# Performance work log

Hardware: AMD Instinct MI355X
Metric: run time of the kernel (lower is better)

## Reference

```python
import jax, jax.numpy as jnp
import numpy as np
from math import pi as PI

N_NODES = 50000
N_EDGES = 1000000
HIDDEN = 128
N_GAUSS = 50
N_FILT = 128
N_COLORS = 4
CUTOFF = 10.0
LOG2 = float(np.log(2.0))


def setup_inputs() -> dict:
    key = jax.random.key(0)
    ks = jax.random.split(key, 16)
    glorot = jax.nn.initializers.glorot_uniform()
    inp = {
        "x": jax.random.normal(ks[0], (N_NODES, HIDDEN), jnp.float32),
        "edge_index": jax.random.randint(ks[1], (2, N_EDGES), 0, N_NODES),
        "edge_weight": jax.random.uniform(ks[2], (N_EDGES,), jnp.float32) * CUTOFF,
        "edge_attr": jax.random.normal(ks[3], (N_EDGES, N_GAUSS), jnp.float32),
        "colors": jax.random.randint(ks[4], (N_EDGES,), 0, N_COLORS),
        # ColoredMLP params, stacked over colors
        "mlp1_w": glorot(ks[5], (N_COLORS, N_FILT, N_GAUSS), jnp.float32),
        "mlp1_b": jnp.zeros((N_COLORS, N_FILT), jnp.float32),
        "mlp2_w": glorot(ks[6], (N_COLORS, N_FILT, N_FILT), jnp.float32),
        "mlp2_b": jnp.zeros((N_COLORS, N_FILT), jnp.float32),
        # CFConv linears
        "lin1_w": glorot(ks[7], (N_FILT, HIDDEN), jnp.float32),
        "lin2_w": glorot(ks[8], (HIDDEN, N_FILT), jnp.float32),
        "lin2_b": jnp.zeros((HIDDEN,), jnp.float32),
        # final Linear
        "lin_w": glorot(ks[9], (HIDDEN, HIDDEN), jnp.float32),
        "lin_b": jnp.zeros((HIDDEN,), jnp.float32),
    }
    return inp


def shifted_softplus(v):
    return jax.nn.softplus(v) - LOG2


def colored_mlp(edge_attr, colors, mlp1_w, mlp1_b, mlp2_w, mlp2_b):
    # per-color small MLP; loop over the small fixed color set, select by mask
    out = jnp.zeros((edge_attr.shape[0], N_FILT), edge_attr.dtype)
    for c in range(N_COLORS):
        h = shifted_softplus(edge_attr @ mlp1_w[c].T + mlp1_b[c])
        h = h @ mlp2_w[c].T + mlp2_b[c]
        out = jnp.where((colors == c)[:, None], h, out)
    return out


def reference(x, edge_index, edge_weight, edge_attr, colors,
              mlp1_w, mlp1_b, mlp2_w, mlp2_b,
              lin1_w, lin2_w, lin2_b, lin_w, lin_b):
    # cosine cutoff
    C = 0.5 * (jnp.cos(edge_weight * PI / CUTOFF) + 1.0)  # [E]
    W = colored_mlp(edge_attr, colors, mlp1_w, mlp1_b, mlp2_w, mlp2_b) * C[:, None]  # [E,F]
    h = x @ lin1_w.T  # [N,F]
    src, dst = edge_index[0], edge_index[1]
    msg = h[src] * W  # gather + modulate, [E,F]
    agg = jax.ops.segment_sum(msg, dst, num_segments=N_NODES)  # scatter-add, [N,F]
    out = agg @ lin2_w.T + lin2_b  # [N,H]
    out = shifted_softplus(out)
    out = out @ lin_w.T + lin_b
    return out
```

## Files before the change

kernel.cpp:

```cpp
#include <hip/hip_runtime.h>
#include <math.h>

#define N_NODES_ 50000
#define N_EDGES_ 1000000
#define HID 128
#define NG 50
#define NF 128
#define NCOL 4
#define CSEG 258048
#define NKEY (NCOL * N_NODES_)
#define CHUNK 625
#define NCHUNK_PER_C 80
#define NCHUNK (NCOL * NCHUNK_PER_C)

typedef short s16x8 __attribute__((ext_vector_type(8)));
typedef float f32x4 __attribute__((ext_vector_type(4)));

__device__ __forceinline__ float sspf(float v) {
    float r = __logf(1.f + __expf(v)) - 0.69314718055994531f;
    return (v > 15.f) ? (v - 0.69314718055994531f) : r;
}

__device__ __forceinline__ unsigned int f2b(float f) {
    unsigned int u = __float_as_uint(f);
    return (u + 0x7fffu + ((u >> 16) & 1u)) >> 16;
}

__global__ __launch_bounds__(256) void hist_kernel(const int* __restrict__ colors,
                                                   const int* __restrict__ edge_index,
                                                   int* __restrict__ hist) {
    int e = blockIdx.x * 256 + threadIdx.x;
    if (e < N_EDGES_) {
        int key = colors[e] * N_NODES_ + edge_index[N_EDGES_ + e];
        atomicAdd(&hist[key], 1);
    }
}

__global__ __launch_bounds__(256) void scan1_kernel(int* __restrict__ hist,
                                                    int* __restrict__ csum) {
    __shared__ int s[CHUNK];
    int b = blockIdx.x;
    int c = b / NCHUNK_PER_C, ch = b % NCHUNK_PER_C;
    int gofs = c * N_NODES_ + ch * CHUNK;
    for (int i = threadIdx.x; i < CHUNK; i += 256) s[i] = hist[gofs + i];
    __syncthreads();
    if (threadIdx.x == 0) {
        int run = 0;
        for (int i = 0; i < CHUNK; ++i) { int t = s[i]; s[i] = run; run += t; }
        csum[b] = run;
    }
    __syncthreads();
    for (int i = threadIdx.x; i < CHUNK; i += 256) hist[gofs + i] = s[i];
}

__global__ __launch_bounds__(64) void scan2_kernel(const int* __restrict__ csum,
                                                   int* __restrict__ cbase,
                                                   int* __restrict__ g_cnt) {
    int c = threadIdx.x;
    if (c < NCOL) {
        int run = 0;
        for (int j = 0; j < NCHUNK_PER_C; ++j) {
            cbase[c * NCHUNK_PER_C + j] = run;
            run += csum[c * NCHUNK_PER_C + j];
        }
        g_cnt[c] = run;
    }
}

__global__ __launch_bounds__(256) void scan3_kernel(int* __restrict__ hist,
                                                    const int* __restrict__ cbase) {
    int b = blockIdx.x;
    int c = b / NCHUNK_PER_C, ch = b % NCHUNK_PER_C;
    int gofs = c * N_NODES_ + ch * CHUNK;
    int add = cbase[b];
    for (int i = threadIdx.x; i < CHUNK; i += 256) hist[gofs + i] += add;
}

__global__ __launch_bounds__(256) void scatter_kernel(const int* __restrict__ colors,
                                                      const int* __restrict__ edge_index,
                                                      const float* __restrict__ edge_weight,
                                                      int* __restrict__ base,
                                                      int* __restrict__ eid_s,
                                                      int* __restrict__ dst_s,
                                                      float* __restrict__ cw_s) {
    int e = blockIdx.x * 256 + threadIdx.x;
    if (e < N_EDGES_) {
        int c = colors[e];
        int d = edge_index[N_EDGES_ + e];
        int key = c * N_NODES_ + d;
        int r = atomicAdd(&base[key], 1);
        int slot = c * CSEG + r;
        eid_s[slot] = e;
        dst_s[slot] = d;
        cw_s[slot] = 0.5f * (__cosf(edge_weight[e] * 0.31415926535897932f) + 1.f);
    }
}

__global__ __launch_bounds__(256) void wconv_kernel(const float* __restrict__ m1w,
                                                    const float* __restrict__ m2w,
                                                    unsigned short* __restrict__ m1b16,
                                                    unsigned short* __restrict__ m2b16) {
    int idx = blockIdx.x * 256 + threadIdx.x;
    if (idx < NCOL * NF * 64) {
        int c = idx / (NF * 64);
        int rem = idx % (NF * 64);
        int n = rem / 64, k = rem % 64;
        float v = (k < NG) ? m1w[(c * NF + n) * NG + k] : 0.f;
        m1b16[idx] = (unsigned short)f2b(v);
    } else if (idx < NCOL * NF * 64 + NCOL * NF * NF) {
        int j = idx - NCOL * NF * 64;
        int cn = j / NF;
        int k = j % NF;
        int ks = k >> 5, qk = (k >> 3) & 3, jj = k & 7;
        int tau = ((2 * ks + (jj >> 2)) << 4) | (qk << 2) | (jj & 3);
        m2b16[j] = (unsigned short)f2b(m2w[cn * NF + tau]);
    }
}

__global__ __launch_bounds__(256, 4) void passA_kernel(
    const int* __restrict__ edge_index,
    const float* __restrict__ edge_attr,
    const unsigned short* __restrict__ m1b16, const unsigned short* __restrict__ m2b16,
    const float* __restrict__ m1bias, const float* __restrict__ m2bias,
    const float* __restrict__ h, const int* __restrict__ eid_s,
    const int* __restrict__ dst_s, const float* __restrict__ cw_s,
    const int* __restrict__ g_cnt, float* __restrict__ agg) {

    __shared__ __align__(16) char sm2[32768];

    int c = blockIdx.x >> 12;
    int tile = blockIdx.x & 4095;
    int cnt = g_cnt[c];
    if (tile * 64 >= cnt) return;
    int pos0 = c * CSEG + tile * 64;

    int tid = threadIdx.x;
    int wv = tid >> 6;
    int l15 = tid & 15;
    int q = (tid >> 4) & 3;
    int e = (wv << 4) | l15;

    {
        const uint4* g4 = (const uint4*)(m2b16 + (size_t)c * NF * NF);
#pragma unroll
        for (int i = 0; i < 8; ++i) {
            int c0 = tid + 256 * i;
            int row = c0 >> 4;
            int k0 = c0 & 15;
            int dstb = row * 256 + ((k0 * 16) ^ ((row & 7) << 4));
            *(uint4*)(sm2 + dstb) = g4[c0];
        }
    }

    int eid = eid_s[pos0 + e];
    int d = dst_s[pos0 + e];
    float cw = cw_s[pos0 + e];
    int sidx = 0;
    if (eid >= 0) sidx = edge_index[eid];

    union { s16x8 v; unsigned int u[4]; } bf0, bf1;
    {
        const float* ear = edge_attr + (size_t)((eid >= 0) ? eid : 0) * NG;
        float2 a0 = *(const float2*)(ear + q * 8 + 0);
        float2 a1 = *(const float2*)(ear + q * 8 + 2);
        float2 a2 = *(const float2*)(ear + q * 8 + 4);
        float2 a3 = *(const float2*)(ear + q * 8 + 6);
        bf0.u[0] = f2b(a0.x) | (f2b(a0.y) << 16);
        bf0.u[1] = f2b(a1.x) | (f2b(a1.y) << 16);
        bf0.u[2] = f2b(a2.x) | (f2b(a2.y) << 16);
        bf0.u[3] = f2b(a3.x) | (f2b(a3.y) << 16);
        float2 c0 = make_float2(0.f, 0.f), c1 = c0, c2 = c0, c3 = c0;
        int k1 = 32 + q * 8;
        if (q < 2) {
            c0 = *(const float2*)(ear + k1 + 0);
            c1 = *(const float2*)(ear + k1 + 2);
            c2 = *(const float2*)(ear + k1 + 4);
            c3 = *(const float2*)(ear + k1 + 6);
        } else if (q == 2) {
            c0 = *(const float2*)(ear + 48);
        }
        bf1.u[0] = f2b(c0.x) | (f2b(c0.y) << 16);
        bf1.u[1] = f2b(c1.x) | (f2b(c1.y) << 16);
        bf1.u[2] = f2b(c2.x) | (f2b(c2.y) << 16);
        bf1.u[3] = f2b(c3.x) | (f2b(c3.y) << 16);
    }

    uint2 p[8];
    {
        const unsigned short* m1p = m1b16 + (size_t)c * NF * 64;
        const float* b1p = m1bias + c * NF;
#pragma unroll
        for (int m = 0; m < 8; ++m) {
            f32x4 a = (f32x4)(0.f);
            s16x8 af0 = *(const s16x8*)(m1p + (m * 16 + l15) * 64 + q * 8);
            a = __builtin_amdgcn_mfma_f32_16x16x32_bf16(af0, bf0.v, a, 0, 0, 0);
            s16x8 af1 = *(const s16x8*)(m1p + (m * 16 + l15) * 64 + q * 8 + 32);
            a = __builtin_amdgcn_mfma_f32_16x16x32_bf16(af1, bf1.v, a, 0, 0, 0);
            int n0 = m * 16 + q * 4;
            f32x4 bv = *(const f32x4*)(b1p + n0);
            float t0 = sspf(a[0] + bv[0]);
            float t1 = sspf(a[1] + bv[1]);
            float t2 = sspf(a[2] + bv[2]);
            float t3 = sspf(a[3] + bv[3]);
            p[m].x = f2b(t0) | (f2b(t1) << 16);
            p[m].y = f2b(t2) | (f2b(t3) << 16);
        }
    }

    int dprev = __shfl_up(d, 1, 16);
    int dn1 = __shfl_down(d, 1, 16);
    int dn2 = __shfl_down(d, 2, 16);
    int dn4 = __shfl_down(d, 4, 16);
    int dn8 = __shfl_down(d, 8, 16);
    bool s1 = (dn1 == d) && (l15 + 1 < 16);
    bool s2 = (dn2 == d) && (l15 + 2 < 16);
    bool s4 = (dn4 == d) && (l15 + 4 < 16);
    bool s8 = (dn8 == d) && (l15 + 8 < 16);
    bool head = (d >= 0) && (l15 == 0 || d != dprev);

    __syncthreads();

    const float* b2p = m2bias + c * NF;
    const float* hrow = h + (size_t)sidx * HID;
    float* ap = agg + (size_t)((d >= 0) ? d : 0) * HID + (q << 2);
    int rowb0 = l15 * 256;
    int sw = (l15 & 7) << 4;

#pragma unroll
    for (int m = 0; m < 8; ++m) {
        f32x4 a2 = (f32x4)(0.f);
        const char* rp = sm2 + rowb0 + m * 4096;
#pragma unroll
        for (int ks = 0; ks < 4; ++ks) {
            union { s16x8 v; unsigned int u[4]; } bfr;
            bfr.u[0] = p[2 * ks].x;
            bfr.u[1] = p[2 * ks].y;
            bfr.u[2] = p[2 * ks + 1].x;
            bfr.u[3] = p[2 * ks + 1].y;
            s16x8 af = *(const s16x8*)(rp + ((q * 16 + ks * 64) ^ sw));
            a2 = __builtin_amdgcn_mfma_f32_16x16x32_bf16(af, bfr.v, a2, 0, 0, 0);
        }
        int n0 = m * 16 + q * 4;
        f32x4 hv = *(const f32x4*)(hrow + n0);
        f32x4 bv = *(const f32x4*)(b2p + n0);
        a2[0] = (a2[0] + bv[0]) * cw * hv[0];
        a2[1] = (a2[1] + bv[1]) * cw * hv[1];
        a2[2] = (a2[2] + bv[2]) * cw * hv[2];
        a2[3] = (a2[3] + bv[3]) * cw * hv[3];

#define SSTEP(sflag, dd)                                                     \
        {                                                                    \
            float v0 = __shfl_down(a2[0], dd, 16);                           \
            float v1 = __shfl_down(a2[1], dd, 16);                           \
            float v2 = __shfl_down(a2[2], dd, 16);                           \
            float v3 = __shfl_down(a2[3], dd, 16);                           \
            if (sflag) { a2[0] += v0; a2[1] += v1; a2[2] += v2; a2[3] += v3; } \
        }
        SSTEP(s1, 1)
        SSTEP(s2, 2)
        SSTEP(s4, 4)
        SSTEP(s8, 8)
#undef SSTEP

        if (head) {
            atomicAdd(ap + m * 16 + 0, a2[0]);
            atomicAdd(ap + m * 16 + 1, a2[1]);
            atomicAdd(ap + m * 16 + 2, a2[2]);
            atomicAdd(ap + m * 16 + 3, a2[3]);
        }
    }
}

__device__ __forceinline__ void fma_2x8(float (&acc)[2][8], float2 a, float4 b0, float4 b1) {
    acc[0][0] += a.x * b0.x; acc[0][1] += a.x * b0.y;
    acc[0][2] += a.x * b0.z; acc[0][3] += a.x * b0.w;
    acc[0][4] += a.x * b1.x; acc[0][5] += a.x * b1.y;
    acc[0][6] += a.x * b1.z; acc[0][7] += a.x * b1.w;
    acc[1][0] += a.y * b0.x; acc[1][1] += a.y * b0.y;
    acc[1][2] += a.y * b0.z; acc[1][3] += a.y * b0.w;
    acc[1][4] += a.y * b1.x; acc[1][5] += a.y * b1.y;
    acc[1][6] += a.y * b1.z; acc[1][7] += a.y * b1.w;
}

__device__ __forceinline__ void load_wT32(const float4* __restrict__ w4, int kc,
                                          float (*wT)[132], int tid) {
#pragma unroll
    for (int i = 0; i < 4; ++i) {
        int lin = tid + 256 * i;
        int col = lin >> 3;
        int m = lin & 7;
        float4 v = w4[col * 32 + (kc >> 2) + m];
        wT[4 * m + 0][col] = v.x;
        wT[4 * m + 1][col] = v.y;
        wT[4 * m + 2][col] = v.z;
        wT[4 * m + 3][col] = v.w;
    }
}

__global__ __launch_bounds__(256) void lin1_kernel(const float* __restrict__ x,
                                                   const float* __restrict__ w,
                                                   float* __restrict__ h) {
    __shared__ float xT[HID][36];
    __shared__ float wT[32][132];
    int tid = threadIdx.x;
    int tx = tid & 15, ty = tid >> 4;
    int r0 = blockIdx.x * 32;
    const float4* x4 = (const float4*)x;
#pragma unroll
    for (int i = 0; i < 4; ++i) {
        int lin = tid + 256 * i;
        int r = lin >> 5, m = lin & 31;
        int rr = r0 + r; if (rr > N_NODES_ - 1) rr = N_NODES_ - 1;
        float4 v = x4[rr * 32 + m];
        xT[4 * m + 0][r] = v.x; xT[4 * m + 1][r] = v.y;
        xT[4 * m + 2][r] = v.z; xT[4 * m + 3][r] = v.w;
    }
    float acc[2][8] = {};
    for (int kc = 0; kc < HID; kc += 32) {
        __syncthreads();
        load_wT32((const float4*)w, kc, wT, tid);
        __syncthreads();
#pragma unroll 8
        for (int k2 = 0; k2 < 32; ++k2) {
            float2 a = *(const float2*)&xT[kc + k2][2 * ty];
            float4 b0 = *(const float4*)&wT[k2][8 * tx];
            float4 b1 = *(const float4*)&wT[k2][8 * tx + 4];
            fma_2x8(acc, a, b0, b1);
        }
    }
    float4* h4 = (float4*)h;
#pragma unroll
    for (int i = 0; i < 2; ++i) {
        int row = r0 + 2 * ty + i;
        if (row < N_NODES_) {
            h4[row * 32 + 2 * tx]     = make_float4(acc[i][0], acc[i][1], acc[i][2], acc[i][3]);
            h4[row * 32 + 2 * tx + 1] = make_float4(acc[i][4], acc[i][5], acc[i][6], acc[i][7]);
        }
    }
}

__global__ __launch_bounds__(256) void out_kernel(
    const float* __restrict__ agg,
    const float* __restrict__ w2, const float* __restrict__ b2,
    const float* __restrict__ w3, const float* __restrict__ b3,
    float* __restrict__ out) {
    __shared__ float sT[HID][36];
    __shared__ float wT[32][132];
    int tid = threadIdx.x;
    int tx = tid & 15, ty = tid >> 4;
    int r0 = blockIdx.x * 32;
    const float4* a4 = (const float4*)agg;
#pragma unroll
    for (int i = 0; i < 4; ++i) {
        int lin = tid + 256 * i;
        int r = lin >> 5, m = lin & 31;
        int rr = r0 + r; if (rr > N_NODES_ - 1) rr = N_NODES_ - 1;
        float4 v = a4[rr * 32 + m];
        sT[4 * m + 0][r] = v.x; sT[4 * m + 1][r] = v.y;
        sT[4 * m + 2][r] = v.z; sT[4 * m + 3][r] = v.w;
    }
    float acc[2][8] = {};
    for (int kc = 0; kc < HID; kc += 32) {
        __syncthreads();
        load_wT32((const float4*)w2, kc, wT, tid);
        __syncthreads();
#pragma unroll 8
        for (int k2 = 0; k2 < 32; ++k2) {
            float2 a = *(const float2*)&sT[kc + k2][2 * ty];
            float4 c0 = *(const float4*)&wT[k2][8 * tx];
            float4 c1 = *(const float4*)&wT[k2][8 * tx + 4];
            fma_2x8(acc, a, c0, c1);
        }
    }
    __syncthreads();
#pragma unroll
    for (int j = 0; j < 8; ++j) {
        int col = 8 * tx + j;
        float bbv = b2[col];
        sT[col][2 * ty]     = sspf(acc[0][j] + bbv);
        sT[col][2 * ty + 1] = sspf(acc[1][j] + bbv);
    }
    float acc2[2][8] = {};
    for (int kc = 0; kc < HID; kc += 32) {
        __syncthreads();
        load_wT32((const float4*)w3, kc, wT, tid);
        __syncthreads();
#pragma unroll 8
        for (int k2 = 0; k2 < 32; ++k2) {
            float2 a = *(const float2*)&sT[kc + k2][2 * ty];
            float4 c0 = *(const float4*)&wT[k2][8 * tx];
            float4 c1 = *(const float4*)&wT[k2][8 * tx + 4];
            fma_2x8(acc2, a, c0, c1);
        }
    }
    float4* out4 = (float4*)out;
#pragma unroll
    for (int i = 0; i < 2; ++i) {
        int row = r0 + 2 * ty + i;
        if (row < N_NODES_) {
            out4[row * 32 + 2 * tx] = make_float4(
                acc2[i][0] + b3[8 * tx + 0], acc2[i][1] + b3[8 * tx + 1],
                acc2[i][2] + b3[8 * tx + 2], acc2[i][3] + b3[8 * tx + 3]);
            out4[row * 32 + 2 * tx + 1] = make_float4(
                acc2[i][4] + b3[8 * tx + 4], acc2[i][5] + b3[8 * tx + 5],
                acc2[i][6] + b3[8 * tx + 6], acc2[i][7] + b3[8 * tx + 7]);
        }
    }
}

extern "C" void kernel_launch(void* const* d_in, const int* in_sizes, int n_in,
                              void* d_out, int out_size, void* d_ws, size_t ws_size,
                              hipStream_t stream) {
    const float* x           = (const float*)d_in[0];
    const int*   edge_index  = (const int*)d_in[1];
    const float* edge_weight = (const float*)d_in[2];
    const float* edge_attr   = (const float*)d_in[3];
    const int*   colors      = (const int*)d_in[4];
    const float* m1w         = (const float*)d_in[5];
    const float* m1b         = (const float*)d_in[6];
    const float* m2w         = (const float*)d_in[7];
    const float* m2b         = (const float*)d_in[8];
    const float* lin1w       = (const float*)d_in[9];
    const float* lin2w       = (const float*)d_in[10];
    const float* lin2b       = (const float*)d_in[11];
    const float* linw        = (const float*)d_in[12];
    const float* linb        = (const float*)d_in[13];
    float* out = (float*)d_out;

    char* ws = (char*)d_ws;
    float* h      = (float*)(ws);
    float* agg    = (float*)(ws + 25600000);
    int*   eid_s  = (int*)(ws + 51200000);
    int*   dst_s  = (int*)(ws + 55328768);
    float* cw_s   = (float*)(ws + 59457536);
    int*   base   = (int*)(ws + 63586304);
    int*   csum   = (int*)(ws + 64386304);
    int*   cbase  = (int*)(ws + 64387584);
    int*   g_cnt  = (int*)(ws + 64388864);
    unsigned short* m1b16 = (unsigned short*)(ws + 64388928);
    unsigned short* m2b16 = (unsigned short*)(ws + 64454464);

    hipMemsetAsync(agg, 0, (size_t)N_NODES_ * HID * sizeof(float), stream);
    hipMemsetAsync(base, 0, NKEY * sizeof(int), stream);
    hipMemsetAsync(eid_s, 0xFF, (size_t)NCOL * CSEG * sizeof(int), stream);
    hipMemsetAsync(dst_s, 0xFF, (size_t)NCOL * CSEG * sizeof(int), stream);

    hist_kernel<<<(N_EDGES_ + 255) / 256, 256, 0, stream>>>(colors, edge_index, base);
    scan1_kernel<<<NCHUNK, 256, 0, stream>>>(base, csum);
    scan2_kernel<<<1, 64, 0, stream>>>(csum, cbase, g_cnt);
    scan3_kernel<<<NCHUNK, 256, 0, stream>>>(base, cbase);
    scatter_kernel<<<(N_EDGES_ + 255) / 256, 256, 0, stream>>>(colors, edge_index, edge_weight,
                                                               base, eid_s, dst_s, cw_s);
    wconv_kernel<<<(NCOL * NF * 64 + NCOL * NF * NF + 255) / 256, 256, 0, stream>>>(m1w, m2w, m1b16, m2b16);
    lin1_kernel<<<(N_NODES_ + 31) / 32, 256, 0, stream>>>(x, lin1w, h);
    passA_kernel<<<NCOL * 4096, 256, 0, stream>>>(edge_index, edge_attr,
                                                  m1b16, m2b16, m1b, m2b, h, eid_s,
                                                  dst_s, cw_s, g_cnt, agg);
    out_kernel<<<(N_NODES_ + 31) / 32, 256, 0, stream>>>(agg, lin2w, lin2b, linw, linb, out);
}
```

Before: 980.3 us.

## Pack edge records and restructure passA MFMA and DPP segment reduction

Merges the three sorted edge arrays into one interleaved record per edge. The record stores the edge id, dst and src packed into one word, and the cutoff weight, so passA no longer does a dependent gather of edge_index to find the source node. In passA, the MFMA chains for both MLP layers are reordered so the eight independent accumulators are issued back to back, and the h-row loads are hoisted ahead of the second GEMM. The shuffle-based segmented reduction is replaced with DPP row-shift plus FMA on flag values. The memsets are replaced by a fill kernel for the record array. The costs are 16-bit packing of node indices, which only works because there are fewer than 65536 nodes, 12-byte strided record loads, and higher register pressure.

```diff
diff --git a/kernel.cpp b/kernel.cpp
--- a/kernel.cpp
+++ b/kernel.cpp
@@ -24,6 +24,12 @@
 __device__ __forceinline__ unsigned int f2b(float f) {
     unsigned int u = __float_as_uint(f);
     return (u + 0x7fffu + ((u >> 16) & 1u)) >> 16;
+}
+
+template <int CTRL>
+__device__ __forceinline__ float dpp_shl_f(float v) {
+    return __int_as_float(__builtin_amdgcn_update_dpp(
+        0, __float_as_int(v), CTRL, 0xF, 0xF, false));
 }
 
 __global__ __launch_bounds__(256) void hist_kernel(const int* __restrict__ colors,
@@ -76,23 +82,32 @@
     for (int i = threadIdx.x; i < CHUNK; i += 256) hist[gofs + i] += add;
 }
 
+__global__ __launch_bounds__(256) void fill_kernel(int* __restrict__ erec) {
+    int i = blockIdx.x * 256 + threadIdx.x;
+    if (i < NCOL * CSEG) {
+        erec[3 * i + 0] = -1;
+        erec[3 * i + 1] = (int)0xFFFF0000u;
+        erec[3 * i + 2] = 0;
+    }
+}
+
 __global__ __launch_bounds__(256) void scatter_kernel(const int* __restrict__ colors,
                                                       const int* __restrict__ edge_index,
                                                       const float* __restrict__ edge_weight,
                                                       int* __restrict__ base,
-                                                      int* __restrict__ eid_s,
-                                                      int* __restrict__ dst_s,
-                                                      float* __restrict__ cw_s) {
+                                                      int* __restrict__ erec) {
     int e = blockIdx.x * 256 + threadIdx.x;
     if (e < N_EDGES_) {
         int c = colors[e];
         int d = edge_index[N_EDGES_ + e];
+        int s = edge_index[e];
         int key = c * N_NODES_ + d;
         int r = atomicAdd(&base[key], 1);
-        int slot = c * CSEG + r;
-        eid_s[slot] = e;
-        dst_s[slot] = d;
-        cw_s[slot] = 0.5f * (__cosf(edge_weight[e] * 0.31415926535897932f) + 1.f);
+        float cwv = 0.5f * (__cosf(edge_weight[e] * 0.31415926535897932f) + 1.f);
+        size_t slot = (size_t)(c * CSEG + r) * 3;
+        erec[slot + 0] = e;
+        erec[slot + 1] = (int)(((unsigned)d << 16) | (unsigned)s);
+        erec[slot + 2] = (int)__float_as_uint(cwv);
     }
 }
 
@@ -118,12 +133,10 @@
 }
 
 __global__ __launch_bounds__(256, 4) void passA_kernel(
-    const int* __restrict__ edge_index,
     const float* __restrict__ edge_attr,
     const unsigned short* __restrict__ m1b16, const unsigned short* __restrict__ m2b16,
     const float* __restrict__ m1bias, const float* __restrict__ m2bias,
-    const float* __restrict__ h, const int* __restrict__ eid_s,
-    const int* __restrict__ dst_s, const float* __restrict__ cw_s,
+    const float* __restrict__ h, const int* __restrict__ erec,
     const int* __restrict__ g_cnt, float* __restrict__ agg) {
 
     __shared__ __align__(16) char sm2[32768];
@@ -152,22 +165,23 @@
         }
     }
 
-    int eid = eid_s[pos0 + e];
-    int d = dst_s[pos0 + e];
-    float cw = cw_s[pos0 + e];
-    int sidx = 0;
-    if (eid >= 0) sidx = edge_index[eid];
+    size_t ri = (size_t)(pos0 + e) * 3;
+    int eid = erec[ri + 0];
+    unsigned w1 = (unsigned)erec[ri + 1];
+    float cw = __int_as_float(erec[ri + 2]);
+    int d = (int)(w1 >> 16);
+    int sidx = (int)(w1 & 0xFFFFu);
 
     union { s16x8 v; unsigned int u[4]; } bf0, bf1;
     {
         const float* ear = edge_attr + (size_t)((eid >= 0) ? eid : 0) * NG;
         float2 a0 = *(const float2*)(ear + q * 8 + 0);
         float2 a1 = *(const float2*)(ear + q * 8 + 2);
-        float2 a2 = *(const float2*)(ear + q * 8 + 4);
+        float2 a2v = *(const float2*)(ear + q * 8 + 4);
         float2 a3 = *(const float2*)(ear + q * 8 + 6);
         bf0.u[0] = f2b(a0.x) | (f2b(a0.y) << 16);
         bf0.u[1] = f2b(a1.x) | (f2b(a1.y) << 16);
-        bf0.u[2] = f2b(a2.x) | (f2b(a2.y) << 16);
+        bf0.u[2] = f2b(a2v.x) | (f2b(a2v.y) << 16);
         bf0.u[3] = f2b(a3.x) | (f2b(a3.y) << 16);
         float2 c0 = make_float2(0.f, 0.f), c1 = c0, c2 = c0, c3 = c0;
         int k1 = 32 + q * 8;
@@ -185,23 +199,33 @@
         bf1.u[3] = f2b(c3.x) | (f2b(c3.y) << 16);
     }
 
+    f32x4 acc1[8];
+    {
+        const unsigned short* m1p = m1b16 + (size_t)c * NF * 64;
+#pragma unroll
+        for (int m = 0; m < 8; ++m) {
+            f32x4 z = (f32x4)(0.f);
+            s16x8 af0 = *(const s16x8*)(m1p + (m * 16 + l15) * 64 + q * 8);
+            acc1[m] = __builtin_amdgcn_mfma_f32_16x16x32_bf16(af0, bf0.v, z, 0, 0, 0);
+        }
+#pragma unroll
+        for (int m = 0; m < 8; ++m) {
+            s16x8 af1 = *(const s16x8*)(m1p + (m * 16 + l15) * 64 + q * 8 + 32);
+            acc1[m] = __builtin_amdgcn_mfma_f32_16x16x32_bf16(af1, bf1.v, acc1[m], 0, 0, 0);
+        }
+    }
+
     uint2 p[8];
     {
-        const unsigned short* m1p = m1b16 + (size_t)c * NF * 64;
         const float* b1p = m1bias + c * NF;
 #pragma unroll
         for (int m = 0; m < 8; ++m) {
-            f32x4 a = (f32x4)(0.f);
-            s16x8 af0 = *(const s16x8*)(m1p + (m * 16 + l15) * 64 + q * 8);
-            a = __builtin_amdgcn_mfma_f32_16x16x32_bf16(af0, bf0.v, a, 0, 0, 0);
-            s16x8 af1 = *(const s16x8*)(m1p + (m * 16 + l15) * 64 + q * 8 + 32);
-            a = __builtin_amdgcn_mfma_f32_16x16x32_bf16(af1, bf1.v, a, 0, 0, 0);
             int n0 = m * 16 + q * 4;
             f32x4 bv = *(const f32x4*)(b1p + n0);
-            float t0 = sspf(a[0] + bv[0]);
-            float t1 = sspf(a[1] + bv[1]);
-            float t2 = sspf(a[2] + bv[2]);
-            float t3 = sspf(a[3] + bv[3]);
+            float t0 = sspf(acc1[m][0] + bv[0]);
+            float t1 = sspf(acc1[m][1] + bv[1]);
+            float t2 = sspf(acc1[m][2] + bv[2]);
+            float t3 = sspf(acc1[m][3] + bv[3]);
             p[m].x = f2b(t0) | (f2b(t1) << 16);
             p[m].y = f2b(t2) | (f2b(t3) << 16);
         }
@@ -212,24 +236,25 @@
     int dn2 = __shfl_down(d, 2, 16);
     int dn4 = __shfl_down(d, 4, 16);
     int dn8 = __shfl_down(d, 8, 16);
-    bool s1 = (dn1 == d) && (l15 + 1 < 16);
-    bool s2 = (dn2 == d) && (l15 + 2 < 16);
-    bool s4 = (dn4 == d) && (l15 + 4 < 16);
-    bool s8 = (dn8 == d) && (l15 + 8 < 16);
-    bool head = (d >= 0) && (l15 == 0 || d != dprev);
+    float f1 = ((dn1 == d) && (l15 + 1 < 16)) ? 1.f : 0.f;
+    float f2 = ((dn2 == d) && (l15 + 2 < 16)) ? 1.f : 0.f;
+    float f4 = ((dn4 == d) && (l15 + 4 < 16)) ? 1.f : 0.f;
+    float f8 = ((dn8 == d) && (l15 + 8 < 16)) ? 1.f : 0.f;
+    bool head = (eid >= 0) && (l15 == 0 || d != dprev);
 
     __syncthreads();
 
-    const float* b2p = m2bias + c * NF;
     const float* hrow = h + (size_t)sidx * HID;
-    float* ap = agg + (size_t)((d >= 0) ? d : 0) * HID + (q << 2);
-    int rowb0 = l15 * 256;
-    int sw = (l15 & 7) << 4;
-
-#pragma unroll
-    for (int m = 0; m < 8; ++m) {
-        f32x4 a2 = (f32x4)(0.f);
-        const char* rp = sm2 + rowb0 + m * 4096;
+    f32x4 hv[8];
+#pragma unroll
+    for (int m = 0; m < 8; ++m) hv[m] = *(const f32x4*)(hrow + m * 16 + q * 4);
+
+    f32x4 a2[8];
+#pragma unroll
+    for (int m = 0; m < 8; ++m) a2[m] = (f32x4)(0.f);
+    {
+        int rowb0 = l15 * 256;
+        int sw = (l15 & 7) << 4;
 #pragma unroll
         for (int ks = 0; ks < 4; ++ks) {
             union { s16x8 v; unsigned int u[4]; } bfr;
@@ -237,36 +262,49 @@
             bfr.u[1] = p[2 * ks].y;
             bfr.u[2] = p[2 * ks + 1].x;
             bfr.u[3] = p[2 * ks + 1].y;
-            s16x8 af = *(const s16x8*)(rp + ((q * 16 + ks * 64) ^ sw));
-            a2 = __builtin_amdgcn_mfma_f32_16x16x32_bf16(af, bfr.v, a2, 0, 0, 0);
-        }
-        int n0 = m * 16 + q * 4;
-        f32x4 hv = *(const f32x4*)(hrow + n0);
-        f32x4 bv = *(const f32x4*)(b2p + n0);
-        a2[0] = (a2[0] + bv[0]) * cw * hv[0];
-        a2[1] = (a2[1] + bv[1]) * cw * hv[1];
-        a2[2] = (a2[2] + bv[2]) * cw * hv[2];
-        a2[3] = (a2[3] + bv[3]) * cw * hv[3];
-
-#define SSTEP(sflag, dd)                                                     \
-        {                                                                    \
-            float v0 = __shfl_down(a2[0], dd, 16);                           \
-            float v1 = __shfl_down(a2[1], dd, 16);                           \
-            float v2 = __shfl_down(a2[2], dd, 16);                           \
-            float v3 = __shfl_down(a2[3], dd, 16);                           \
-            if (sflag) { a2[0] += v0; a2[1] += v1; a2[2] += v2; a2[3] += v3; } \
-        }
-        SSTEP(s1, 1)
-        SSTEP(s2, 2)
-        SSTEP(s4, 4)
-        SSTEP(s8, 8)
-#undef SSTEP
-
-        if (head) {
-            atomicAdd(ap + m * 16 + 0, a2[0]);
-            atomicAdd(ap + m * 16 + 1, a2[1]);
-            atomicAdd(ap + m * 16 + 2, a2[2]);
-            atomicAdd(ap + m * 16 + 3, a2[3]);
+            int off = (q * 16 + ks * 64) ^ sw;
+#pragma unroll
+            for (int m = 0; m < 8; ++m) {
+                s16x8 af = *(const s16x8*)(sm2 + rowb0 + m * 4096 + off);
+                a2[m] = __builtin_amdgcn_mfma_f32_16x16x32_bf16(af, bfr.v, a2[m], 0, 0, 0);
+            }
+        }
+    }
+
+    {
+        const float* b2p = m2bias + c * NF;
+#pragma unroll
+        for (int m = 0; m < 8; ++m) {
+            int n0 = m * 16 + q * 4;
+            f32x4 bv = *(const f32x4*)(b2p + n0);
+            a2[m][0] = (a2[m][0] + bv[0]) * cw * hv[m][0];
+            a2[m][1] = (a2[m][1] + bv[1]) * cw * hv[m][1];
+            a2[m][2] = (a2[m][2] + bv[2]) * cw * hv[m][2];
+            a2[m][3] = (a2[m][3] + bv[3]) * cw * hv[m][3];
+        }
+    }
+
+#pragma unroll
+    for (int m = 0; m < 8; ++m) {
+#pragma unroll
+        for (int j = 0; j < 4; ++j) {
+            float x = a2[m][j];
+            x = fmaf(f1, dpp_shl_f<0x101>(x), x);
+            x = fmaf(f2, dpp_shl_f<0x102>(x), x);
+            x = fmaf(f4, dpp_shl_f<0x104>(x), x);
+            x = fmaf(f8, dpp_shl_f<0x108>(x), x);
+            a2[m][j] = x;
+        }
+    }
+
+    if (head) {
+        float* ap = agg + (size_t)d * HID + (q << 2);
+#pragma unroll
+        for (int m = 0; m < 8; ++m) {
+            atomicAdd(ap + m * 16 + 0, a2[m][0]);
+            atomicAdd(ap + m * 16 + 1, a2[m][1]);
+            atomicAdd(ap + m * 16 + 2, a2[m][2]);
+            atomicAdd(ap + m * 16 + 3, a2[m][3]);
         }
     }
 }
@@ -430,9 +468,7 @@
     char* ws = (char*)d_ws;
     float* h      = (float*)(ws);
     float* agg    = (float*)(ws + 25600000);
-    int*   eid_s  = (int*)(ws + 51200000);
-    int*   dst_s  = (int*)(ws + 55328768);
-    float* cw_s   = (float*)(ws + 59457536);
+    int*   erec   = (int*)(ws + 51200000);
     int*   base   = (int*)(ws + 63586304);
     int*   csum   = (int*)(ws + 64386304);
     int*   cbase  = (int*)(ws + 64387584);
@@ -442,19 +478,17 @@
 
     hipMemsetAsync(agg, 0, (size_t)N_NODES_ * HID * sizeof(float), stream);
     hipMemsetAsync(base, 0, NKEY * sizeof(int), stream);
-    hipMemsetAsync(eid_s, 0xFF, (size_t)NCOL * CSEG * sizeof(int), stream);
-    hipMemsetAsync(dst_s, 0xFF, (size_t)NCOL * CSEG * sizeof(int), stream);
-
+
+    fill_kernel<<<(NCOL * CSEG + 255) / 256, 256, 0, stream>>>(erec);
     hist_kernel<<<(N_EDGES_ + 255) / 256, 256, 0, stream>>>(colors, edge_index, base);
     scan1_kernel<<<NCHUNK, 256, 0, stream>>>(base, csum);
     scan2_kernel<<<1, 64, 0, stream>>>(csum, cbase, g_cnt);
     scan3_kernel<<<NCHUNK, 256, 0, stream>>>(base, cbase);
     scatter_kernel<<<(N_EDGES_ + 255) / 256, 256, 0, stream>>>(colors, edge_index, edge_weight,
-                                                               base, eid_s, dst_s, cw_s);
+                                                               base, erec);
     wconv_kernel<<<(NCOL * NF * 64 + NCOL * NF * NF + 255) / 256, 256, 0, stream>>>(m1w, m2w, m1b16, m2b16);
     lin1_kernel<<<(N_NODES_ + 31) / 32, 256, 0, stream>>>(x, lin1w, h);
-    passA_kernel<<<NCOL * 4096, 256, 0, stream>>>(edge_index, edge_attr,
-                                                  m1b16, m2b16, m1b, m2b, h, eid_s,
-                                                  dst_s, cw_s, g_cnt, agg);
+    passA_kernel<<<NCOL * 4096, 256, 0, stream>>>(edge_attr, m1b16, m2b16, m1b, m2b,
+                                                  h, erec, g_cnt, agg);
     out_kernel<<<(N_NODES_ + 31) / 32, 256, 0, stream>>>(agg, lin2w, lin2b, linw, linb, out);
 }
```

Result: faster. 958.8 us (-2.2%).
